# Performance work log

Hardware: AMD Instinct MI355X
Metric: run time of the kernel (lower is better)

## Reference

```python
import jax, jax.numpy as jnp
import numpy as np

# Transformer config constants (from init_kwargs)
SRF = 3.0                 # spatial_receptive_field
SRF2 = SRF * SRF
ALPHA = 2.0
BETA = 8.0
GAMMA = 16.0
RES = jnp.array([0.5, 0.5, 0.5], dtype=jnp.float32)   # relative_positional_gresolution
N_BUCKETS = 2 * 8 + 1                                  # 2*beta + 1 = 17
MUL = jnp.array([N_BUCKETS ** 2, N_BUCKETS, 1], dtype=jnp.float32)  # [289,17,1]
SLICES_PER_ROT = 2


def setup_inputs() -> dict:
    key = jax.random.key(0)
    k1, k2 = jax.random.split(key)
    N = 3072
    # LiDAR-like point coordinates in a 10m cube; receptive field 3.0 makes radius filter selective
    xyz = jax.random.uniform(k1, (N, 3), dtype=jnp.float32) * 10.0
    # grid columns: [batch, block, gx, gy, gz]; values < 128 per the torch assert
    grid = jax.random.randint(k2, (N, 5), 0, 8, dtype=jnp.int32)
    return {"xyz": xyz, "grid": grid}


def _bucket_base(x):
    # from_dxyz_to_bucket_base, res.size(0)==3 branch
    x = x / RES
    x_abs = jnp.abs(x)
    log_ratio = jnp.log(jnp.maximum(x_abs, 1e-6) / ALPHA) / np.log(GAMMA / ALPHA)
    sup = jnp.minimum(jnp.round(ALPHA - (BETA - ALPHA) * log_ratio), BETA)
    sup = jnp.sign(x) * sup
    return BETA + jnp.where(x_abs <= ALPHA, jnp.round(x), sup)


def reference(xyz, grid):
    # no-kvp path of jit_compute_interactions, expressed as dense [N,N] pair masks
    batch = grid[:, 0]
    block = grid[:, 1]
    coords = grid[:, 2:]            # grid_look[:, 1:]

    # batch equality filter (meshgrid + batch==batch)
    batch_eq = batch[:, None] == batch[None, :]
    # causal block filter: block[iq] <= block[ik]
    block_le = block[:, None] <= block[None, :]

    # force_keep_neighbours: adjacent voxels within the same block
    coord_adj = jnp.max(jnp.abs(coords[:, None, :] - coords[None, :, :]), axis=-1) <= 1
    forcekeep = coord_adj & (block[:, None] == block[None, :])

    # coarse spatial hash on xy: ceil(xy / srf), neighbor cells only
    xy_coarse = jnp.ceil(xyz[:, :2] / SRF).astype(jnp.int32)
    keep_coarse = jnp.max(jnp.abs(xy_coarse[:, None, :] - xy_coarse[None, :, :]), axis=-1) <= 1

    # pairwise deltas (torch uses fp16 here; fp32 kept for numerical clarity) [N,N,3]
    dxyz = xyz[:, None, :] - xyz[None, :, :]
    keepr = jnp.sum(dxyz * dxyz, axis=-1) <= SRF2

    mask = batch_eq & block_le & (forcekeep | keep_coarse) & (forcekeep | keepr)

    dxyz_m = jnp.where(mask[..., None], dxyz, 0.0)

    # from_dxyz_to_bucket_mul: log-bucketize each axis, flatten via mul_buckets
    buckets = jnp.sum(MUL * _bucket_base(dxyz_m), axis=-1).astype(jnp.int32)
    buckets = jnp.where(mask, buckets, 0)

    # dscanid = scanid[ik] - scanid[iq], scanid = block // slices_per_rotation
    scanid = block // SLICES_PER_ROT
    dscanid = jnp.where(mask, scanid[None, :] - scanid[:, None], 0)

    return dxyz_m, buckets, dscanid, mask
```

## Files before the change

kernel.cpp:

```cpp
#include <hip/hip_runtime.h>
#include <cmath>


#define TPB 256
#define JB  1024
#define II  6

typedef float f32x4 __attribute__((ext_vector_type(4)));

__device__ __forceinline__ float bucket_base(float v) {
    const float x  = v * 2.0f;
    const float xa = fabsf(x);
    if (xa <= 2.0f) {
        return 8.0f + rintf(x);
    }
    const float lr = logf(fmaxf(xa, 1e-6f) * 0.5f) / 2.0794415416798357f;
    const float sup = fminf(rintf(2.0f - 6.0f * lr), 8.0f);
    return 8.0f + ((x > 0.0f) ? sup : -sup);
}

__global__ __launch_bounds__(256) void pair_kernel(
    const float* __restrict__ xyz, const int* __restrict__ grid,
    float* __restrict__ out, int N) {
#pragma clang fp contract(off)
    __shared__ float s_st[3 * JB];

    const int tid = threadIdx.x;
    const int w   = tid >> 6;
    const int l   = tid & 63;
    const int jw0 = 256 * w;
    const int J0  = blockIdx.x * JB;
    const int I0  = blockIdx.y * II;

    float jx[4], jy[4], jz[4];
    int   jbat[4], jblk[4], jc0[4], jc1[4], jc2[4], xcj[4], ycj[4];
#pragma unroll
    for (int k = 0; k < 4; ++k) {
        const int j = J0 + jw0 + 64 * k + l;
        jx[k]   = xyz[3 * j + 0];
        jy[k]   = xyz[3 * j + 1];
        jz[k]   = xyz[3 * j + 2];
        jbat[k] = grid[5 * j + 0];
        jblk[k] = grid[5 * j + 1];
        jc0[k]  = grid[5 * j + 2];
        jc1[k]  = grid[5 * j + 3];
        jc2[k]  = grid[5 * j + 4];
        xcj[k] = (int)ceilf(jx[k] / 3.0f);
        ycj[k] = (int)ceilf(jy[k] / 3.0f);
    }

    const size_t NN = (size_t)N * (size_t)N;

    for (int ii = 0; ii < II; ++ii) {
        const int i = I0 + ii;
        if (i >= N) break;

        const float xi = xyz[3 * i + 0];
        const float yi = xyz[3 * i + 1];
        const float zi = xyz[3 * i + 2];
        const int bat_i = grid[5 * i + 0];
        const int blk_i = grid[5 * i + 1];
        const int c0i = grid[5 * i + 2];
        const int c1i = grid[5 * i + 3];
        const int c2i = grid[5 * i + 4];
        const int xci = (int)ceilf(xi / 3.0f);
        const int yci = (int)ceilf(yi / 3.0f);
        const int scan_i = blk_i >> 1;

        float dxm[4], dym[4], dzm[4];
        bool  mk[4];
        bool  any = false;
#pragma unroll
        for (int k = 0; k < 4; ++k) {
            const float dx = xi - jx[k];
            const float dy = yi - jy[k];
            const float dz = zi - jz[k];
            const bool batch_eq = (bat_i == jbat[k]);
            const bool block_le = (blk_i <= jblk[k]);
            const int  cadj = max(max(abs(c0i - jc0[k]), abs(c1i - jc1[k])),
                                  abs(c2i - jc2[k]));
            const bool forcekeep = (cadj <= 1) && (blk_i == jblk[k]);
            const bool keep_coarse =
                max(abs(xci - xcj[k]), abs(yci - ycj[k])) <= 1;
            const float d2 = dx * dx + dy * dy + dz * dz;
            const bool keepr = (d2 <= 9.0f);
            const bool m = batch_eq && block_le &&
                           (forcekeep || keep_coarse) && (forcekeep || keepr);
            mk[k] = m;
            any |= m;
            dxm[k] = m ? dx : 0.0f;
            dym[k] = m ? dy : 0.0f;
            dzm[k] = m ? dz : 0.0f;
        }

        const size_t rowbase = (size_t)i * (size_t)N + (size_t)J0;
        float* __restrict__ obkt = out + NN * 3 + rowbase;
        float* __restrict__ odsc = out + NN * 4 + rowbase;
        float* __restrict__ omsk = out + NN * 5 + rowbase;
        f32x4* __restrict__ od4 =
            reinterpret_cast<f32x4*>(out + 3 * (rowbase + (size_t)jw0));
        f32x4* __restrict__ ob4 = reinterpret_cast<f32x4*>(obkt + jw0);
        f32x4* __restrict__ os4 = reinterpret_cast<f32x4*>(odsc + jw0);
        f32x4* __restrict__ om4 = reinterpret_cast<f32x4*>(omsk + jw0);

        if (__ballot(any ? 1 : 0) == 0ULL) {
            const f32x4 z4 = {0.0f, 0.0f, 0.0f, 0.0f};
#pragma unroll
            for (int p = 0; p < 3; ++p)
                __builtin_nontemporal_store(z4, od4 + 64 * p + l);
            __builtin_nontemporal_store(z4, ob4 + l);
            __builtin_nontemporal_store(z4, os4 + l);
            __builtin_nontemporal_store(z4, om4 + l);
            continue;
        }

#pragma unroll
        for (int k = 0; k < 4; ++k) {
            const int jl = jw0 + 64 * k + l;
            float b = 0.0f, d = 0.0f, mvf = 0.0f;
            if (mk[k]) {
                const float b0 = bucket_base(dxm[k]);
                const float b1 = bucket_base(dym[k]);
                const float b2 = bucket_base(dzm[k]);
                const float bsum = (289.0f * b0 + 17.0f * b1) + b2;
                b   = (float)(int)bsum;
                d   = (float)((jblk[k] >> 1) - scan_i);
                mvf = 1.0f;
            }
            __builtin_nontemporal_store(b,   obkt + jl);
            __builtin_nontemporal_store(d,   odsc + jl);
            __builtin_nontemporal_store(mvf, omsk + jl);
            s_st[3 * jl + 0] = dxm[k];
            s_st[3 * jl + 1] = dym[k];
            s_st[3 * jl + 2] = dzm[k];
        }

        const f32x4* st4 = reinterpret_cast<const f32x4*>(s_st + 3 * jw0);
#pragma unroll
        for (int p = 0; p < 3; ++p)
            __builtin_nontemporal_store(st4[64 * p + l], od4 + 64 * p + l);
    }
}

extern "C" void kernel_launch(void* const* d_in, const int* in_sizes, int n_in,
                              void* d_out, int out_size, void* d_ws, size_t ws_size,
                              hipStream_t stream) {
    const float* xyz  = (const float*)d_in[0];
    const int*   grid = (const int*)d_in[1];
    float*       out  = (float*)d_out;
    const int N = in_sizes[0] / 3;

    dim3 gdim(N / JB, (N + II - 1) / II, 1);
    pair_kernel<<<gdim, dim3(TPB, 1, 1), 0, stream>>>(xyz, grid, out, N);
}
```

Before: 232.7 us.

## Split output into bulk zero-fill kernel plus sparse masked-pair writes

Adds a separate grid-stride kernel that zero-fills the entire output buffer. The pair kernel then writes only the entries whose mask is set, dropping the shared-memory staging and the dense nontemporal stores, and the row tile grows from 6 to 12. The aim is to replace per-tile mask-dependent dense writes with a simple streaming memset followed by sparse scatter. In exchange it adds a second launch, the full buffer is still written, the scattered scalar stores are poorly coalesced, and the i<N guard is removed, which assumes N is divisible by 12.

After: 246.7 us. 1.06x slower.

```diff
diff --git a/kernel.cpp b/kernel.cpp
--- a/kernel.cpp
+++ b/kernel.cpp
@@ -4,7 +4,7 @@
 
 #define TPB 256
 #define JB  1024
-#define II  6
+#define II  12
 
 typedef float f32x4 __attribute__((ext_vector_type(4)));
 
@@ -19,12 +19,20 @@
     return 8.0f + ((x > 0.0f) ? sup : -sup);
 }
 
-__global__ __launch_bounds__(256) void pair_kernel(
+__global__ __launch_bounds__(256) void zero_kernel(float* __restrict__ out,
+                                                   size_t nvec4) {
+    f32x4* o = reinterpret_cast<f32x4*>(out);
+    const f32x4 z = {0.0f, 0.0f, 0.0f, 0.0f};
+    const size_t stride = (size_t)gridDim.x * blockDim.x;
+    for (size_t v = (size_t)blockIdx.x * blockDim.x + threadIdx.x; v < nvec4;
+         v += stride)
+        o[v] = z;
+}
+
+__global__ __launch_bounds__(256) void pair_sparse_kernel(
     const float* __restrict__ xyz, const int* __restrict__ grid,
     float* __restrict__ out, int N) {
 #pragma clang fp contract(off)
-    __shared__ float s_st[3 * JB];
-
     const int tid = threadIdx.x;
     const int w   = tid >> 6;
     const int l   = tid & 63;
@@ -45,15 +53,14 @@
         jc0[k]  = grid[5 * j + 2];
         jc1[k]  = grid[5 * j + 3];
         jc2[k]  = grid[5 * j + 4];
-        xcj[k] = (int)ceilf(jx[k] / 3.0f);
-        ycj[k] = (int)ceilf(jy[k] / 3.0f);
+        xcj[k]  = (int)ceilf(jx[k] / 3.0f);
+        ycj[k]  = (int)ceilf(jy[k] / 3.0f);
     }
 
     const size_t NN = (size_t)N * (size_t)N;
 
     for (int ii = 0; ii < II; ++ii) {
         const int i = I0 + ii;
-        if (i >= N) break;
 
         const float xi = xyz[3 * i + 0];
         const float yi = xyz[3 * i + 1];
@@ -88,57 +95,29 @@
                            (forcekeep || keep_coarse) && (forcekeep || keepr);
             mk[k] = m;
             any |= m;
-            dxm[k] = m ? dx : 0.0f;
-            dym[k] = m ? dy : 0.0f;
-            dzm[k] = m ? dz : 0.0f;
+            dxm[k] = dx;
+            dym[k] = dy;
+            dzm[k] = dz;
         }
 
-        const size_t rowbase = (size_t)i * (size_t)N + (size_t)J0;
-        float* __restrict__ obkt = out + NN * 3 + rowbase;
-        float* __restrict__ odsc = out + NN * 4 + rowbase;
-        float* __restrict__ omsk = out + NN * 5 + rowbase;
-        f32x4* __restrict__ od4 =
-            reinterpret_cast<f32x4*>(out + 3 * (rowbase + (size_t)jw0));
-        f32x4* __restrict__ ob4 = reinterpret_cast<f32x4*>(obkt + jw0);
-        f32x4* __restrict__ os4 = reinterpret_cast<f32x4*>(odsc + jw0);
-        f32x4* __restrict__ om4 = reinterpret_cast<f32x4*>(omsk + jw0);
-
-        if (__ballot(any ? 1 : 0) == 0ULL) {
-            const f32x4 z4 = {0.0f, 0.0f, 0.0f, 0.0f};
-#pragma unroll
-            for (int p = 0; p < 3; ++p)
-                __builtin_nontemporal_store(z4, od4 + 64 * p + l);
-            __builtin_nontemporal_store(z4, ob4 + l);
-            __builtin_nontemporal_store(z4, os4 + l);
-            __builtin_nontemporal_store(z4, om4 + l);
-            continue;
-        }
+        if (__ballot(any ? 1 : 0) == 0ULL) continue;
 
 #pragma unroll
         for (int k = 0; k < 4; ++k) {
-            const int jl = jw0 + 64 * k + l;
-            float b = 0.0f, d = 0.0f, mvf = 0.0f;
-            if (mk[k]) {
-                const float b0 = bucket_base(dxm[k]);
-                const float b1 = bucket_base(dym[k]);
-                const float b2 = bucket_base(dzm[k]);
-                const float bsum = (289.0f * b0 + 17.0f * b1) + b2;
-                b   = (float)(int)bsum;
-                d   = (float)((jblk[k] >> 1) - scan_i);
-                mvf = 1.0f;
-            }
-            __builtin_nontemporal_store(b,   obkt + jl);
-            __builtin_nontemporal_store(d,   odsc + jl);
-            __builtin_nontemporal_store(mvf, omsk + jl);
-            s_st[3 * jl + 0] = dxm[k];
-            s_st[3 * jl + 1] = dym[k];
-            s_st[3 * jl + 2] = dzm[k];
+            if (!mk[k]) continue;
+            const int j = J0 + jw0 + 64 * k + l;
+            const size_t base = (size_t)i * (size_t)N + (size_t)j;
+            out[3 * base + 0] = dxm[k];
+            out[3 * base + 1] = dym[k];
+            out[3 * base + 2] = dzm[k];
+            const float b0 = bucket_base(dxm[k]);
+            const float b1 = bucket_base(dym[k]);
+            const float b2 = bucket_base(dzm[k]);
+            const float bsum = (289.0f * b0 + 17.0f * b1) + b2;
+            out[NN * 3 + base] = (float)(int)bsum;
+            out[NN * 4 + base] = (float)((jblk[k] >> 1) - scan_i);
+            out[NN * 5 + base] = 1.0f;
         }
-
-        const f32x4* st4 = reinterpret_cast<const f32x4*>(s_st + 3 * jw0);
-#pragma unroll
-        for (int p = 0; p < 3; ++p)
-            __builtin_nontemporal_store(st4[64 * p + l], od4 + 64 * p + l);
     }
 }
 
@@ -150,6 +129,11 @@
     float*       out  = (float*)d_out;
     const int N = in_sizes[0] / 3;
 
-    dim3 gdim(N / JB, (N + II - 1) / II, 1);
-    pair_kernel<<<gdim, dim3(TPB, 1, 1), 0, stream>>>(xyz, grid, out, N);
+    const size_t NN = (size_t)N * (size_t)N;
+    const size_t nvec4 = NN * 6 / 4;
+
+    zero_kernel<<<dim3(2048, 1, 1), dim3(TPB, 1, 1), 0, stream>>>(out, nvec4);
+
+    dim3 gdim(N / JB, N / II, 1);
+    pair_sparse_kernel<<<gdim, dim3(TPB, 1, 1), 0, stream>>>(xyz, grid, out, N);
 }
```
